# Optimization experiments

Measured on AMD Instinct MI355X. Metric: run time of the kernel, lower is better.

## Reference

```python
import jax, jax.numpy as jnp
import numpy as np

B, F, E, T = 4, 128, 3000, 6000  # batch, features, input edges, unroll_target


def setup_inputs() -> dict:
    key = jax.random.key(0)
    k1, k2 = jax.random.split(key)
    features = jax.random.normal(k1, (B, F, E), dtype=jnp.float32)
    # Sparse one-hot-like group matrix: each padded group matrix is binary with
    # a few nonzeros per target column (as produced by mesh.get_groups + pad_groups).
    unroll_mat = (jax.random.uniform(k2, (B, E, T)) < (2.0 / E)).astype(jnp.float32)
    # occurrences[b, t] = number of times target edge t occurs across groups;
    # pad_occurrences pads with 1, so clamp to a minimum of 1.
    occurrences = jnp.maximum(unroll_mat.sum(axis=1), 1.0)  # (B, T)
    return {"features": features, "unroll_mat": unroll_mat, "occurrences": occurrences}


def reference(features, unroll_mat, occurrences):
    # unroll_mat: (B, E, T) padded group matrix; occurrences: (B, T)
    # normalized mapping, then dense bmm: (B,F,E) @ (B,E,T) -> (B,F,T)
    norm_mat = unroll_mat / occurrences[:, None, :]
    return jnp.einsum('bfe,bet->bft', features, norm_mat)
```

## Files before the change

### kernel.cpp

```cpp
#include <hip/hip_runtime.h>

#define B 4
#define F 128
#define E 3000
#define T 6000
#define K 16
#define ECHUNK 40
#define CAP 1024

__global__ __launch_bounds__(256) void feat_transpose_kernel(
        const float* __restrict__ features, float* __restrict__ ft,
        int* __restrict__ counts) {
    __shared__ float tile[32][33];
    const int b  = blockIdx.z;
    const int e0 = blockIdx.x * 32;
    const int f0 = blockIdx.y * 32;
    const int tx = threadIdx.x;
    const int ty = threadIdx.y;

    {
        const int blk = (blockIdx.z * gridDim.y + blockIdx.y) * gridDim.x + blockIdx.x;
        const int gtid = blk * 256 + ty * 32 + tx;
        if (gtid < B * T) counts[gtid] = 0;
    }

    const float* fb = features + (size_t)b * F * E;
    float* ob = ft + (size_t)b * E * F;
#pragma unroll
    for (int j = 0; j < 4; ++j) {
        const int f = f0 + ty + 8 * j;
        const int e = e0 + tx;
        tile[ty + 8 * j][tx] = (e < E) ? fb[(size_t)f * E + e] : 0.0f;
    }
    __syncthreads();
#pragma unroll
    for (int j = 0; j < 4; ++j) {
        const int e = e0 + ty + 8 * j;
        const int f = f0 + tx;
        if (e < E) ob[(size_t)e * F + f] = tile[tx][ty + 8 * j];
    }
}

__global__ __launch_bounds__(256) void unpool_scan_kernel(
        const float* __restrict__ unroll,
        int* __restrict__ counts,
        int* __restrict__ idx) {
    __shared__ int ls_cnt;
    __shared__ int2 ls_buf[CAP];

    const int b  = blockIdx.z;
    const int e0 = blockIdx.y * ECHUNK;
    const int t4 = (blockIdx.x * blockDim.x + threadIdx.x) * 4;
    const bool active = (t4 + 3) < T;

    if (threadIdx.x == 0) ls_cnt = 0;
    __syncthreads();

    const float* base = unroll + (size_t)b * E * T + t4;
    int* cbase = counts + b * T;
    int* ibase = idx + (size_t)b * T * K;

    if (active) {
#define LROW(e) (*reinterpret_cast<const float4*>(base + (size_t)(e) * T))
#define ANY_NZ(v) ((__float_as_uint(v.x) | __float_as_uint(v.y) | \
                    __float_as_uint(v.z) | __float_as_uint(v.w)) != 0u)
#define PROC(v, ee)                                                                  \
    do {                                                                             \
        if (__ballot(ANY_NZ(v))) {                                                   \
            if (v.x != 0.0f) { int s = atomicAdd(&ls_cnt, 1); if (s < CAP) ls_buf[s] = make_int2(t4 + 0, (ee)); } \
            if (v.y != 0.0f) { int s = atomicAdd(&ls_cnt, 1); if (s < CAP) ls_buf[s] = make_int2(t4 + 1, (ee)); } \
            if (v.z != 0.0f) { int s = atomicAdd(&ls_cnt, 1); if (s < CAP) ls_buf[s] = make_int2(t4 + 2, (ee)); } \
            if (v.w != 0.0f) { int s = atomicAdd(&ls_cnt, 1); if (s < CAP) ls_buf[s] = make_int2(t4 + 3, (ee)); } \
        }                                                                            \
    } while (0)

        float4 c0 = LROW(e0 + 0), c1 = LROW(e0 + 1), c2 = LROW(e0 + 2), c3 = LROW(e0 + 3);
#pragma unroll 1
        for (int eg = 0; eg < ECHUNK - 4; eg += 4) {
            const int e = e0 + eg;
            float4 n0 = LROW(e + 4), n1 = LROW(e + 5), n2 = LROW(e + 6), n3 = LROW(e + 7);
            PROC(c0, e + 0);
            PROC(c1, e + 1);
            PROC(c2, e + 2);
            PROC(c3, e + 3);
            c0 = n0; c1 = n1; c2 = n2; c3 = n3;
        }
        const int el = e0 + ECHUNK - 4;
        PROC(c0, el + 0);
        PROC(c1, el + 1);
        PROC(c2, el + 2);
        PROC(c3, el + 3);
#undef PROC
#undef ANY_NZ
#undef LROW
    }

    __syncthreads();
    const int n = ls_cnt;
    if (n <= CAP) {
        for (int i = threadIdx.x; i < n; i += 256) {
            const int2 p = ls_buf[i];
            const int c = atomicAdd(&cbase[p.x], 1);
            if (c < K) ibase[(size_t)p.x * K + c] = p.y;
        }
    } else if (active) {
        for (int e = e0; e < e0 + ECHUNK; ++e) {
            const float4 v = *reinterpret_cast<const float4*>(base + (size_t)e * T);
            if (v.x != 0.0f) { int c = atomicAdd(&cbase[t4 + 0], 1); if (c < K) ibase[(size_t)(t4 + 0) * K + c] = e; }
            if (v.y != 0.0f) { int c = atomicAdd(&cbase[t4 + 1], 1); if (c < K) ibase[(size_t)(t4 + 1) * K + c] = e; }
            if (v.z != 0.0f) { int c = atomicAdd(&cbase[t4 + 2], 1); if (c < K) ibase[(size_t)(t4 + 2) * K + c] = e; }
            if (v.w != 0.0f) { int c = atomicAdd(&cbase[t4 + 3], 1); if (c < K) ibase[(size_t)(t4 + 3) * K + c] = e; }
        }
    }
}

__global__ __launch_bounds__(256) void unpool_gather_kernel(
        const float* __restrict__ ft,
        const float* __restrict__ occ,
        const float* __restrict__ unroll,
        const int* __restrict__ counts,
        const int* __restrict__ idx,
        float* __restrict__ out) {
    const int b  = blockIdx.z;
    const int t  = blockIdx.x * 256 + threadIdx.x;
    const int f0 = blockIdx.y * 16;
    if (t >= T) return;

    const int c = counts[b * T + t];
    const float inv = 1.0f / occ[b * T + t];
    const float* fb = ft + (size_t)b * E * F;
    float* ob = out + (size_t)b * F * T + t;

    if (c <= K) {
        int es[K];
        const int4* ip4 = reinterpret_cast<const int4*>(idx + ((size_t)b * T + t) * K);
#pragma unroll
        for (int q = 0; q < 4; ++q) {
            const int4 v = ip4[q];
            es[4 * q + 0] = v.x; es[4 * q + 1] = v.y;
            es[4 * q + 2] = v.z; es[4 * q + 3] = v.w;
        }
#pragma unroll
        for (int j = 0; j < 4; ++j) {
            const int f = f0 + 4 * j;
            float4 a = make_float4(0.f, 0.f, 0.f, 0.f);
#pragma unroll
            for (int k = 0; k < K; ++k) {
                if (k < c) {
                    const float4 v = *reinterpret_cast<const float4*>(fb + (size_t)es[k] * F + f);
                    a.x += v.x; a.y += v.y; a.z += v.z; a.w += v.w;
                }
            }
            __builtin_nontemporal_store(a.x * inv, ob + (size_t)(f + 0) * T);
            __builtin_nontemporal_store(a.y * inv, ob + (size_t)(f + 1) * T);
            __builtin_nontemporal_store(a.z * inv, ob + (size_t)(f + 2) * T);
            __builtin_nontemporal_store(a.w * inv, ob + (size_t)(f + 3) * T);
        }
    } else {
        for (int j = 0; j < 4; ++j) {
            const int f = f0 + 4 * j;
            float4 a = make_float4(0.f, 0.f, 0.f, 0.f);
            for (int e = 0; e < E; ++e) {
                if (unroll[((size_t)b * E + e) * T + t] != 0.0f) {
                    const float4 v = *reinterpret_cast<const float4*>(fb + (size_t)e * F + f);
                    a.x += v.x; a.y += v.y; a.z += v.z; a.w += v.w;
                }
            }
            ob[(size_t)(f + 0) * T] = a.x * inv;
            ob[(size_t)(f + 1) * T] = a.y * inv;
            ob[(size_t)(f + 2) * T] = a.z * inv;
            ob[(size_t)(f + 3) * T] = a.w * inv;
        }
    }
}

__global__ void unpool_dense_fallback(const float* __restrict__ features,
                                      const float* __restrict__ unroll,
                                      const float* __restrict__ occ,
                                      float* __restrict__ out) {
    const int b = blockIdx.z;
    const int f = blockIdx.y;
    const int t = blockIdx.x * 64 + threadIdx.x;
    if (t >= T) return;
    const float* frow = features + ((size_t)b * F + f) * E;
    const float* ub = unroll + (size_t)b * E * T;
    float acc = 0.0f;
    for (int e = 0; e < E; ++e) acc += frow[e] * ub[(size_t)e * T + t];
    out[((size_t)b * F + f) * T + t] = acc / occ[b * T + t];
}

extern "C" void kernel_launch(void* const* d_in, const int* in_sizes, int n_in,
                              void* d_out, int out_size, void* d_ws, size_t ws_size,
                              hipStream_t stream) {
    const float* features = (const float*)d_in[0];
    const float* unroll   = (const float*)d_in[1];
    const float* occ      = (const float*)d_in[2];
    float* out = (float*)d_out;

    const size_t counts_bytes = (size_t)B * T * sizeof(int);
    const size_t idx_bytes    = (size_t)B * T * K * sizeof(int);
    const size_t ft_bytes     = (size_t)B * E * F * sizeof(float);

    if (ws_size < counts_bytes + idx_bytes + ft_bytes) {
        dim3 g((T + 63) / 64, F, B);
        unpool_dense_fallback<<<g, 64, 0, stream>>>(features, unroll, occ, out);
        return;
    }

    int*   counts = (int*)d_ws;
    int*   idx    = counts + (size_t)B * T;
    float* ft     = (float*)(idx + (size_t)B * T * K);

    dim3 gt((E + 31) / 32, F / 32, B);
    feat_transpose_kernel<<<gt, dim3(32, 8), 0, stream>>>(features, ft, counts);

    dim3 g1((T / 4 + 255) / 256, E / ECHUNK, B);
    unpool_scan_kernel<<<g1, 256, 0, stream>>>(unroll, counts, idx);

    dim3 g2((T + 255) / 256, F / 16, B);
    unpool_gather_kernel<<<g2, 256, 0, stream>>>(ft, occ, unroll, counts, idx, out);
}
```

Measured before the change: 71.36 us.

## Scan unroll matrix row-per-wavefront and halve feature tile in gather

The sparse scan now gives each 64-lane wavefront one full row of the unroll matrix, issuing 8 float4 loads in flight per lane across 24 column chunks, instead of column tiles over 40-row chunks. This targets the streaming read of the large dense unroll matrix, which dominates the traffic, by improving contiguity and memory-level parallelism. The gather kernel also processes 8 features per thread instead of 16, which doubles the grid for more parallelism but re-reads the index lists twice as often.

New measurement: 69.54 us. -2.6%, faster.

```diff
diff --git a/kernel.cpp b/kernel.cpp
--- a/kernel.cpp
+++ b/kernel.cpp
@@ -5,7 +5,6 @@
 #define E 3000
 #define T 6000
 #define K 16
-#define ECHUNK 40
 #define CAP 1024
 
 __global__ __launch_bounds__(256) void feat_transpose_kernel(
@@ -41,59 +40,49 @@
     }
 }
 
-__global__ __launch_bounds__(256) void unpool_scan_kernel(
+__global__ __launch_bounds__(256) void unpool_scan_rows(
         const float* __restrict__ unroll,
         int* __restrict__ counts,
         int* __restrict__ idx) {
     __shared__ int ls_cnt;
     __shared__ int2 ls_buf[CAP];
 
-    const int b  = blockIdx.z;
-    const int e0 = blockIdx.y * ECHUNK;
-    const int t4 = (blockIdx.x * blockDim.x + threadIdx.x) * 4;
-    const bool active = (t4 + 3) < T;
+    const int rid  = blockIdx.x * 4 + (threadIdx.x >> 6);
+    const int lane = threadIdx.x & 63;
+    const int b = rid / E;
+    const int e = rid % E;
+    const float* row = unroll + (size_t)rid * T;
 
     if (threadIdx.x == 0) ls_cnt = 0;
     __syncthreads();
 
-    const float* base = unroll + (size_t)b * E * T + t4;
     int* cbase = counts + b * T;
     int* ibase = idx + (size_t)b * T * K;
 
-    if (active) {
-#define LROW(e) (*reinterpret_cast<const float4*>(base + (size_t)(e) * T))
 #define ANY_NZ(v) ((__float_as_uint(v.x) | __float_as_uint(v.y) | \
                     __float_as_uint(v.z) | __float_as_uint(v.w)) != 0u)
-#define PROC(v, ee)                                                                  \
-    do {                                                                             \
-        if (__ballot(ANY_NZ(v))) {                                                   \
-            if (v.x != 0.0f) { int s = atomicAdd(&ls_cnt, 1); if (s < CAP) ls_buf[s] = make_int2(t4 + 0, (ee)); } \
-            if (v.y != 0.0f) { int s = atomicAdd(&ls_cnt, 1); if (s < CAP) ls_buf[s] = make_int2(t4 + 1, (ee)); } \
-            if (v.z != 0.0f) { int s = atomicAdd(&ls_cnt, 1); if (s < CAP) ls_buf[s] = make_int2(t4 + 2, (ee)); } \
-            if (v.w != 0.0f) { int s = atomicAdd(&ls_cnt, 1); if (s < CAP) ls_buf[s] = make_int2(t4 + 3, (ee)); } \
-        }                                                                            \
-    } while (0)
-
-        float4 c0 = LROW(e0 + 0), c1 = LROW(e0 + 1), c2 = LROW(e0 + 2), c3 = LROW(e0 + 3);
+
 #pragma unroll 1
-        for (int eg = 0; eg < ECHUNK - 4; eg += 4) {
-            const int e = e0 + eg;
-            float4 n0 = LROW(e + 4), n1 = LROW(e + 5), n2 = LROW(e + 6), n3 = LROW(e + 7);
-            PROC(c0, e + 0);
-            PROC(c1, e + 1);
-            PROC(c2, e + 2);
-            PROC(c3, e + 3);
-            c0 = n0; c1 = n1; c2 = n2; c3 = n3;
-        }
-        const int el = e0 + ECHUNK - 4;
-        PROC(c0, el + 0);
-        PROC(c1, el + 1);
-        PROC(c2, el + 2);
-        PROC(c3, el + 3);
-#undef PROC
+    for (int c0 = 0; c0 < 24; c0 += 8) {
+        float4 v[8];
+#pragma unroll
+        for (int u = 0; u < 8; ++u) {
+            const int t4 = (c0 + u) * 256 + lane * 4;
+            v[u] = (t4 < T) ? *reinterpret_cast<const float4*>(row + t4)
+                            : make_float4(0.0f, 0.0f, 0.0f, 0.0f);
+        }
+#pragma unroll
+        for (int u = 0; u < 8; ++u) {
+            const int t4 = (c0 + u) * 256 + lane * 4;
+            if (__ballot(ANY_NZ(v[u]))) {
+                if (v[u].x != 0.0f) { int s = atomicAdd(&ls_cnt, 1); if (s < CAP) ls_buf[s] = make_int2(t4 + 0, e); }
+                if (v[u].y != 0.0f) { int s = atomicAdd(&ls_cnt, 1); if (s < CAP) ls_buf[s] = make_int2(t4 + 1, e); }
+                if (v[u].z != 0.0f) { int s = atomicAdd(&ls_cnt, 1); if (s < CAP) ls_buf[s] = make_int2(t4 + 2, e); }
+                if (v[u].w != 0.0f) { int s = atomicAdd(&ls_cnt, 1); if (s < CAP) ls_buf[s] = make_int2(t4 + 3, e); }
+            }
+        }
+    }
 #undef ANY_NZ
-#undef LROW
-    }
 
     __syncthreads();
     const int n = ls_cnt;
@@ -103,9 +92,11 @@
             const int c = atomicAdd(&cbase[p.x], 1);
             if (c < K) ibase[(size_t)p.x * K + c] = p.y;
         }
-    } else if (active) {
-        for (int e = e0; e < e0 + ECHUNK; ++e) {
-            const float4 v = *reinterpret_cast<const float4*>(base + (size_t)e * T);
+    } else {
+        for (int c0 = 0; c0 < 24; ++c0) {
+            const int t4 = c0 * 256 + lane * 4;
+            if (t4 >= T) continue;
+            const float4 v = *reinterpret_cast<const float4*>(row + t4);
             if (v.x != 0.0f) { int c = atomicAdd(&cbase[t4 + 0], 1); if (c < K) ibase[(size_t)(t4 + 0) * K + c] = e; }
             if (v.y != 0.0f) { int c = atomicAdd(&cbase[t4 + 1], 1); if (c < K) ibase[(size_t)(t4 + 1) * K + c] = e; }
             if (v.z != 0.0f) { int c = atomicAdd(&cbase[t4 + 2], 1); if (c < K) ibase[(size_t)(t4 + 2) * K + c] = e; }
@@ -123,7 +114,7 @@
         float* __restrict__ out) {
     const int b  = blockIdx.z;
     const int t  = blockIdx.x * 256 + threadIdx.x;
-    const int f0 = blockIdx.y * 16;
+    const int f0 = blockIdx.y * 8;
     if (t >= T) return;
 
     const int c = counts[b * T + t];
@@ -141,7 +132,7 @@
             es[4 * q + 2] = v.z; es[4 * q + 3] = v.w;
         }
 #pragma unroll
-        for (int j = 0; j < 4; ++j) {
+        for (int j = 0; j < 2; ++j) {
             const int f = f0 + 4 * j;
             float4 a = make_float4(0.f, 0.f, 0.f, 0.f);
 #pragma unroll
@@ -157,7 +148,7 @@
             __builtin_nontemporal_store(a.w * inv, ob + (size_t)(f + 3) * T);
         }
     } else {
-        for (int j = 0; j < 4; ++j) {
+        for (int j = 0; j < 2; ++j) {
             const int f = f0 + 4 * j;
             float4 a = make_float4(0.f, 0.f, 0.f, 0.f);
             for (int e = 0; e < E; ++e) {
@@ -214,9 +205,8 @@
     dim3 gt((E + 31) / 32, F / 32, B);
     feat_transpose_kernel<<<gt, dim3(32, 8), 0, stream>>>(features, ft, counts);
 
-    dim3 g1((T / 4 + 255) / 256, E / ECHUNK, B);
-    unpool_scan_kernel<<<g1, 256, 0, stream>>>(unroll, counts, idx);
-
-    dim3 g2((T + 255) / 256, F / 16, B);
+    unpool_scan_rows<<<(B * E) / 4, 256, 0, stream>>>(unroll, counts, idx);
+
+    dim3 g2((T + 255) / 256, F / 8, B);
     unpool_gather_kernel<<<g2, 256, 0, stream>>>(ft, occ, unroll, counts, idx, out);
 }
```
